# Kernel optimization log

Measured on AMD Instinct MI355X. Metric: run time of the kernel, lower is better.

Reference implementation:

```python
import jax, jax.numpy as jnp
import numpy as np

H = 16          # n_heads
D_MODEL = 1024
DK = D_MODEL // H  # 64
N = 2048        # total tokens (module flattens batch*seq)
NEG = -1000000000.0


def setup_inputs() -> dict:
    key = jax.random.key(0)
    ks = jax.random.split(key, 12)
    s = 1.0 / np.sqrt(D_MODEL)
    inp = {
        "query": jax.random.normal(ks[0], (N, D_MODEL), jnp.float32),
        "key": jax.random.normal(ks[1], (N, D_MODEL), jnp.float32),
        "value": jax.random.normal(ks[2], (N, D_MODEL), jnp.float32),
        "mask": jax.random.randint(ks[3], (1, N), 0, 2, jnp.int32),
        "Wq": jax.random.normal(ks[4], (D_MODEL, D_MODEL), jnp.float32) * s,
        "bq": jax.random.normal(ks[5], (D_MODEL,), jnp.float32) * 0.01,
        "Wk": jax.random.normal(ks[6], (D_MODEL, D_MODEL), jnp.float32) * s,
        "bk": jax.random.normal(ks[7], (D_MODEL,), jnp.float32) * 0.01,
        "Wv": jax.random.normal(ks[8], (D_MODEL, D_MODEL), jnp.float32) * s,
        "bv": jax.random.normal(ks[9], (D_MODEL,), jnp.float32) * 0.01,
        "Wo": jax.random.normal(ks[10], (D_MODEL, D_MODEL), jnp.float32) * s,
        "bo": jax.random.normal(ks[11], (D_MODEL,), jnp.float32) * 0.01,
    }
    return inp


def reference(query, key, value, mask, Wq, bq, Wk, bk, Wv, bv, Wo, bo):
    # Linear projections (torch Linear: x @ W.T + b), then split heads: (N, d_model) -> (h, N, d_k)
    def split_heads(x):
        return x.reshape(-1, H, DK).transpose(1, 0, 2)

    q = split_heads(query @ Wq.T + bq)
    k = split_heads(key @ Wk.T + bk)
    v = split_heads(value @ Wv.T + bv)

    # scaled dot-product attention: scores (h, N, N)
    scores = jnp.einsum("hnd,hmd->hnm", q, k) / jnp.sqrt(jnp.asarray(DK, q.dtype))
    # mask: (1, N) --unsqueeze(1)--> (1, 1, N), broadcast over (h, N, N)
    scores = jnp.where(mask[None, :, :] == 0, jnp.asarray(NEG, scores.dtype), scores)
    p_attn = jax.nn.softmax(scores, axis=-1)  # dropout identity (eval mode)

    x = jnp.einsum("hnm,hmd->hnd", p_attn, v)  # (h, N, d_k)
    x = x.transpose(1, 0, 2).reshape(-1, H * DK)  # (N, d_model)
    out = x @ Wo.T + bo
    return (out, p_attn)
```

## Files before the change

kernel.cpp:

```cpp
#include <hip/hip_runtime.h>


#define NTOK 2048
#define DMODEL 1024
#define NHEAD 16
#define DKH 64

typedef __attribute__((ext_vector_type(8))) short bf16x8;
typedef __attribute__((ext_vector_type(4))) float f32x4;

#define WAITVMC(n)                                          \
  do {                                                      \
    asm volatile("s_waitcnt vmcnt(" n ")" ::: "memory");    \
    __builtin_amdgcn_sched_barrier(0);                      \
  } while (0)
#define BARRIER()                                           \
  do {                                                      \
    __builtin_amdgcn_s_barrier();                           \
    __builtin_amdgcn_sched_barrier(0);                      \
  } while (0)

__device__ __forceinline__ unsigned short f2bf(float x) {
  unsigned int u = __builtin_bit_cast(unsigned int, x);
  u += 0x7fffu + ((u >> 16) & 1u);
  return (unsigned short)(u >> 16);
}

__device__ __forceinline__ void gl16(const void* g, void* l) {
  __builtin_amdgcn_global_load_lds((const __attribute__((address_space(1))) void*)g,
                                   (__attribute__((address_space(3))) void*)l, 16, 0, 0);
}

template<int ROWS>
__device__ __forceinline__ void stage_async(const unsigned short* src, int ld,
                                            char* lds, int w, int lane) {
  constexpr int RPW = ROWS / 4;
#pragma unroll
  for (int i = 0; i < RPW / 8; ++i) {
    const int row = w * RPW + i * 8 + (lane >> 3);
    const unsigned short* g = src + (size_t)row * ld + (((lane & 7) ^ (row & 7)) * 8);
    gl16(g, lds + (size_t)(w * RPW + i * 8) * 128);
  }
}

__device__ __forceinline__ void stage_v(const unsigned short* src, char* lds, int w, int lane) {
#pragma unroll
  for (int i = 0; i < 4; ++i) {
    const int row = w * 16 + i * 4 + (lane >> 4);
    const int ck = lane & 15;
    const unsigned short* g = src + (size_t)row * NTOK + ((ck ^ (row & 7)) * 8);
    gl16(g, lds + (size_t)(w * 16 + i * 4) * 256);
  }
}

__device__ __forceinline__ bf16x8 ldsfrag(const char* lds, int r, int kb) {
  return *(const bf16x8*)(lds + r * 128 + (kb ^ ((r & 7) << 4)));
}
__device__ __forceinline__ bf16x8 ldsfrag256(const char* lds, int r, int kb) {
  return *(const bf16x8*)(lds + r * 256 + (kb ^ ((r & 7) << 4)));
}

struct CvtP {
  const float* src[7];
  unsigned short* dst[7];
  int n8[8];
  const int* mask;
  float* mbias;
};
__global__ __launch_bounds__(256) void cvt_all(CvtP P) {
  const int a = blockIdx.z;
  const int i = blockIdx.x * 256 + threadIdx.x;
  if (i >= P.n8[a]) return;
  if (a == 7) {
#pragma unroll
    for (int r = 0; r < 8; ++r) {
      int j = i * 8 + r;
      P.mbias[j] = P.mask[j] ? 0.0f : -1e30f;
    }
    return;
  }
  const float4* s = (const float4*)P.src[a];
  float4 v0 = s[i * 2], v1 = s[i * 2 + 1];
  ushort4 h0, h1;
  h0.x = f2bf(v0.x); h0.y = f2bf(v0.y); h0.z = f2bf(v0.z); h0.w = f2bf(v0.w);
  h1.x = f2bf(v1.x); h1.y = f2bf(v1.y); h1.z = f2bf(v1.z); h1.w = f2bf(v1.w);
  ((ushort4*)P.dst[a])[i * 2] = h0;
  ((ushort4*)P.dst[a])[i * 2 + 1] = h1;
}

struct GemmP2 {
  const unsigned short* A[3];
  const unsigned short* B[3];
  const float* bias[3];
  unsigned short* Cb16;
  float* Cf32;
  unsigned short* VTd;
  long long sC;
  int lda, ldb, ldc, Nn, K;
};

template<int BM, bool OUTF32, bool VTRANS>
__global__ __launch_bounds__(256) void gemm_glds(GemmP2 P) {
  constexpr int BN = 128, WN = 64, FN = 4;
  constexpr int WM = BM / 2, FM = WM / 16;
  __shared__ char ldsA[BM * 128];
  __shared__ char ldsB[BN * 128];
  const int tid = threadIdx.x;
  const int lane = tid & 63, w = tid >> 6;
  const int l15 = lane & 15, lhi = lane >> 4;
  const int z = blockIdx.z;
  const int zi = (gridDim.z == 3) ? z : 0;
  const int ntn = P.Nn / BN;
  const int m0 = ((int)blockIdx.x / ntn) * BM;
  const int n0 = ((int)blockIdx.x % ntn) * BN;
  const unsigned short* Ab = P.A[zi] + (size_t)m0 * P.lda;
  const unsigned short* Bb = P.B[zi] + (size_t)n0 * P.ldb;
  const int wm = w >> 1, wn = w & 1;

  f32x4 acc[FM][FN] = {};
  for (int k0 = 0; k0 < P.K; k0 += 64) {
    stage_async<BM>(Ab + k0, P.lda, ldsA, w, lane);
    stage_async<BN>(Bb + k0, P.ldb, ldsB, w, lane);
    __syncthreads();
#pragma unroll
    for (int kk = 0; kk < 2; ++kk) {
      const int kb = kk * 64 + lhi * 16;
      bf16x8 a[FM], b[FN];
#pragma unroll
      for (int i = 0; i < FM; ++i) a[i] = ldsfrag(ldsA, wm * WM + i * 16 + l15, kb);
#pragma unroll
      for (int j = 0; j < FN; ++j) b[j] = ldsfrag(ldsB, wn * WN + j * 16 + l15, kb);
#pragma unroll
      for (int i = 0; i < FM; ++i)
#pragma unroll
        for (int j = 0; j < FN; ++j)
          acc[i][j] = __builtin_amdgcn_mfma_f32_16x16x32_bf16(a[i], b[j], acc[i][j], 0, 0, 0);
    }
    __syncthreads();
  }

  const int rbase = m0 + wm * WM + lhi * 4;
  const int cbase = n0 + wn * WN + l15;
  if (VTRANS && z == 2) {
#pragma unroll
    for (int j = 0; j < FN; ++j) {
      const int col = cbase + j * 16;
      const float badd = P.bias[zi][col];
#pragma unroll
      for (int i = 0; i < FM; ++i) {
        ushort4 t;
        t.x = f2bf(acc[i][j][0] + badd); t.y = f2bf(acc[i][j][1] + badd);
        t.z = f2bf(acc[i][j][2] + badd); t.w = f2bf(acc[i][j][3] + badd);
        *(ushort4*)(P.VTd + (size_t)col * NTOK + rbase + i * 16) = t;
      }
    }
    return;
  }
#pragma unroll
  for (int j = 0; j < FN; ++j) {
    const int col = cbase + j * 16;
    const float badd = P.bias[zi] ? P.bias[zi][col] : 0.0f;
#pragma unroll
    for (int i = 0; i < FM; ++i) {
#pragma unroll
      for (int rg = 0; rg < 4; ++rg) {
        const int row = rbase + i * 16 + rg;
        const float v = acc[i][j][rg] + badd;
        if constexpr (OUTF32)
          P.Cf32[(size_t)row * P.ldc + col] = v;
        else
          P.Cb16[(size_t)z * P.sC + (size_t)row * P.ldc + col] = f2bf(v);
      }
    }
  }
}

__global__ __launch_bounds__(256) void attn5(const unsigned short* __restrict__ QP,
                                             const unsigned short* __restrict__ KP,
                                             const unsigned short* __restrict__ VT,
                                             const float* __restrict__ mbias,
                                             float* __restrict__ p,
                                             unsigned short* __restrict__ XB) {
  __shared__ char ldsK[2][128 * 128];
  __shared__ char ldsV[2][64 * 256];
  __shared__ char ldsP[64 * 256];
  const int tid = threadIdx.x;
  const int lane = tid & 63, w = tid >> 6;
  const int l15 = lane & 15, lhi = lane >> 4;
  const int id = blockIdx.x;
  const int h = 2 * (id & 7) + ((id >> 3) & 1);
  const int q0 = (id >> 4) * 64;
  const int mrow = w * 16 + l15;
  constexpr float CEXP = 0.1803368801111204f;

  stage_async<64>(QP + (size_t)q0 * DMODEL + h * DKH, DMODEL, ldsP, w, lane);
  __syncthreads();
  bf16x8 qf0 = ldsfrag(ldsP, mrow, lhi * 16);
  bf16x8 qf1 = ldsfrag(ldsP, mrow, 64 + lhi * 16);

  const unsigned short* Kh = KP + h * DKH;
  const unsigned short* Vh = VT + (size_t)h * DKH * NTOK;

  float rsum = 0.0f;
  stage_async<128>(Kh, DMODEL, ldsK[0], w, lane);
  int b = 0;
  for (int it = 0; it < 16; ++it) {
    WAITVMC("0");
    BARRIER();
    if (it < 15)
      stage_async<128>(Kh + (size_t)(it + 1) * 128 * DMODEL, DMODEL, ldsK[b ^ 1], w, lane);
    __builtin_amdgcn_sched_barrier(0);
    f32x4 sacc[8] = {};
#pragma unroll
    for (int kk = 0; kk < 2; ++kk)
#pragma unroll
      for (int js = 0; js < 8; ++js) {
        bf16x8 kf = ldsfrag(ldsK[b], js * 16 + l15, kk * 64 + lhi * 16);
        sacc[js] = __builtin_amdgcn_mfma_f32_16x16x32_bf16(kf, kk ? qf1 : qf0, sacc[js], 0, 0, 0);
      }
    const float* mb = mbias + it * 128;
#pragma unroll
    for (int js = 0; js < 8; ++js) {
      float4 m4 = *(const float4*)(mb + js * 16 + lhi * 4);
      rsum += exp2f(sacc[js][0] * CEXP + m4.x);
      rsum += exp2f(sacc[js][1] * CEXP + m4.y);
      rsum += exp2f(sacc[js][2] * CEXP + m4.z);
      rsum += exp2f(sacc[js][3] * CEXP + m4.w);
    }
    b ^= 1;
  }
  rsum += __shfl_xor(rsum, 16, 64);
  rsum += __shfl_xor(rsum, 32, 64);
  const float lr = -log2f(rsum);

  f32x4 xacc[4] = {};
  stage_async<128>(Kh, DMODEL, ldsK[0], w, lane);
  stage_v(Vh, ldsV[0], w, lane);
  b = 0;
  for (int it = 0; it < 16; ++it) {
    const int j0 = it * 128;
    if (it == 0) { WAITVMC("0"); } else { WAITVMC("8"); }
    BARRIER();
    if (it < 15) {
      stage_async<128>(Kh + (size_t)(j0 + 128) * DMODEL, DMODEL, ldsK[b ^ 1], w, lane);
      stage_v(Vh + j0 + 128, ldsV[b ^ 1], w, lane);
    }
    __builtin_amdgcn_sched_barrier(0);
    f32x4 sacc[8] = {};
#pragma unroll
    for (int kk = 0; kk < 2; ++kk)
#pragma unroll
      for (int js = 0; js < 8; ++js) {
        bf16x8 kf = ldsfrag(ldsK[b], js * 16 + l15, kk * 64 + lhi * 16);
        sacc[js] = __builtin_amdgcn_mfma_f32_16x16x32_bf16(kf, kk ? qf1 : qf0, sacc[js], 0, 0, 0);
      }
    const float* mb = mbias + j0;
#pragma unroll
    for (int js = 0; js < 8; ++js) {
      float4 m4 = *(const float4*)(mb + js * 16 + lhi * 4);
      ushort4 pb;
      pb.x = f2bf(exp2f(sacc[js][0] * CEXP + (m4.x + lr)));
      pb.y = f2bf(exp2f(sacc[js][1] * CEXP + (m4.y + lr)));
      pb.z = f2bf(exp2f(sacc[js][2] * CEXP + (m4.z + lr)));
      pb.w = f2bf(exp2f(sacc[js][3] * CEXP + (m4.w + lr)));
      *(ushort4*)(ldsP + mrow * 256 + ((js * 32 + lhi * 8) ^ ((mrow & 7) << 4))) = pb;
    }
#pragma unroll
    for (int r = 0; r < 8; ++r) {
      const int row = w * 16 + r * 2 + (lane >> 5);
      const uint2 u =
          *(const uint2*)(ldsP + row * 256 + (((lane & 31) * 8) ^ ((row & 7) << 4)));
      f32x4 f;
      f[0] = __builtin_bit_cast(float, u.x << 16);
      f[1] = __builtin_bit_cast(float, u.x & 0xffff0000u);
      f[2] = __builtin_bit_cast(float, u.y << 16);
      f[3] = __builtin_bit_cast(float, u.y & 0xffff0000u);
      __builtin_nontemporal_store(
          f, (f32x4*)(p + ((size_t)h * NTOK + q0 + row) * NTOK + j0 + (lane & 31) * 4));
    }
#pragma unroll
    for (int jk = 0; jk < 4; ++jk) {
      bf16x8 pf = ldsfrag256(ldsP, mrow, jk * 64 + lhi * 16);
#pragma unroll
      for (int dd = 0; dd < 4; ++dd) {
        bf16x8 vf = ldsfrag256(ldsV[b], dd * 16 + l15, jk * 64 + lhi * 16);
        xacc[dd] = __builtin_amdgcn_mfma_f32_16x16x32_bf16(vf, pf, xacc[dd], 0, 0, 0);
      }
    }
    b ^= 1;
  }

  unsigned short* xrow = XB + (size_t)(q0 + mrow) * DMODEL + h * DKH;
#pragma unroll
  for (int dd = 0; dd < 4; ++dd) {
    ushort4 xb;
    xb.x = f2bf(xacc[dd][0]); xb.y = f2bf(xacc[dd][1]);
    xb.z = f2bf(xacc[dd][2]); xb.w = f2bf(xacc[dd][3]);
    *(ushort4*)(xrow + dd * 16 + lhi * 4) = xb;
  }
}

extern "C" void kernel_launch(void* const* d_in, const int* in_sizes, int n_in,
                              void* d_out, int out_size, void* d_ws, size_t ws_size,
                              hipStream_t stream) {
  (void)in_sizes; (void)n_in; (void)out_size; (void)ws_size;
  const float* query = (const float*)d_in[0];
  const float* key_  = (const float*)d_in[1];
  const float* value = (const float*)d_in[2];
  const int*   mask  = (const int*)d_in[3];
  const float* Wq = (const float*)d_in[4];
  const float* bq = (const float*)d_in[5];
  const float* Wk = (const float*)d_in[6];
  const float* bk = (const float*)d_in[7];
  const float* Wv = (const float*)d_in[8];
  const float* bv = (const float*)d_in[9];
  const float* Wo = (const float*)d_in[10];
  const float* bo = (const float*)d_in[11];

  float* out = (float*)d_out;
  float* p = out + (size_t)NTOK * DMODEL;

  char* ws = (char*)d_ws;
  unsigned short* QP  = (unsigned short*)(ws);
  unsigned short* KP  = (unsigned short*)(ws + (4u << 20));
  unsigned short* VT  = (unsigned short*)(ws + (8u << 20));
  unsigned short* XB  = (unsigned short*)(ws + (12u << 20));
  unsigned short* qB  = (unsigned short*)(ws + (16u << 20));
  unsigned short* kB  = (unsigned short*)(ws + (20u << 20));
  unsigned short* vB  = (unsigned short*)(ws + (24u << 20));
  unsigned short* WqB = (unsigned short*)(ws + (28u << 20));
  unsigned short* WkB = (unsigned short*)(ws + (30u << 20));
  unsigned short* WvB = (unsigned short*)(ws + (32u << 20));
  unsigned short* WoB = (unsigned short*)(ws + (34u << 20));
  float* mbias = (float*)(ws + (36u << 20));

  {
    CvtP C = {};
    C.src[0] = query; C.dst[0] = qB;  C.n8[0] = NTOK * DMODEL / 8;
    C.src[1] = key_;  C.dst[1] = kB;  C.n8[1] = NTOK * DMODEL / 8;
    C.src[2] = value; C.dst[2] = vB;  C.n8[2] = NTOK * DMODEL / 8;
    C.src[3] = Wq;    C.dst[3] = WqB; C.n8[3] = DMODEL * DMODEL / 8;
    C.src[4] = Wk;    C.dst[4] = WkB; C.n8[4] = DMODEL * DMODEL / 8;
    C.src[5] = Wv;    C.dst[5] = WvB; C.n8[5] = DMODEL * DMODEL / 8;
    C.src[6] = Wo;    C.dst[6] = WoB; C.n8[6] = DMODEL * DMODEL / 8;
    C.n8[7] = NTOK / 8;
    C.mask = mask; C.mbias = mbias;
    cvt_all<<<dim3(1024, 1, 8), 256, 0, stream>>>(C);
  }
  {
    GemmP2 P = {};
    P.A[0] = qB; P.A[1] = kB; P.A[2] = vB;
    P.B[0] = WqB; P.B[1] = WkB; P.B[2] = WvB;
    P.bias[0] = bq; P.bias[1] = bk; P.bias[2] = bv;
    P.Cb16 = QP; P.VTd = VT; P.sC = (long long)NTOK * DMODEL;
    P.lda = DMODEL; P.ldb = DMODEL; P.ldc = DMODEL; P.Nn = DMODEL; P.K = DMODEL;
    gemm_glds<128, false, true>
        <<<dim3((NTOK / 128) * (DMODEL / 128), 1, 3), 256, 0, stream>>>(P);
  }
  attn5<<<dim3(512), 256, 0, stream>>>(QP, KP, VT, mbias, p, XB);
  {
    GemmP2 P = {};
    P.A[0] = XB; P.B[0] = WoB; P.bias[0] = bo;
    P.Cf32 = out; P.sC = 0;
    P.lda = DMODEL; P.ldb = DMODEL; P.ldc = DMODEL; P.Nn = DMODEL; P.K = DMODEL;
    gemm_glds<64, true, false>
        <<<dim3((NTOK / 64) * (DMODEL / 128), 1, 1), 256, 0, stream>>>(P);
  }
}
```

Measured before the change: 147.1 us.

## Store attention probabilities directly from registers and prefetch mask bias before MFMAs

The attention kernel now writes the fp32 softmax probabilities straight from the exp results in registers with nontemporal stores. Before, it read bf16 values back from LDS, widened them and wrote coalesced rows. This removes an LDS read pass and stores full-precision probabilities, but each store now covers only 16 bytes per lane across scattered rows, so global coalescing is worse. The mask-bias loads are also hoisted ahead of the MFMA loop so their latency overlaps the matrix math.

```diff
diff --git a/kernel.cpp b/kernel.cpp
--- a/kernel.cpp
+++ b/kernel.cpp
@@ -175,7 +175,7 @@
   }
 }
 
-__global__ __launch_bounds__(256) void attn5(const unsigned short* __restrict__ QP,
+__global__ __launch_bounds__(256) void attn6(const unsigned short* __restrict__ QP,
                                              const unsigned short* __restrict__ KP,
                                              const unsigned short* __restrict__ VT,
                                              const float* __restrict__ mbias,
@@ -210,6 +210,10 @@
     if (it < 15)
       stage_async<128>(Kh + (size_t)(it + 1) * 128 * DMODEL, DMODEL, ldsK[b ^ 1], w, lane);
     __builtin_amdgcn_sched_barrier(0);
+    const float* mb = mbias + it * 128;
+    float4 m4s[8];
+#pragma unroll
+    for (int js = 0; js < 8; ++js) m4s[js] = *(const float4*)(mb + js * 16 + lhi * 4);
     f32x4 sacc[8] = {};
 #pragma unroll
     for (int kk = 0; kk < 2; ++kk)
@@ -218,14 +222,12 @@
         bf16x8 kf = ldsfrag(ldsK[b], js * 16 + l15, kk * 64 + lhi * 16);
         sacc[js] = __builtin_amdgcn_mfma_f32_16x16x32_bf16(kf, kk ? qf1 : qf0, sacc[js], 0, 0, 0);
       }
-    const float* mb = mbias + it * 128;
 #pragma unroll
     for (int js = 0; js < 8; ++js) {
-      float4 m4 = *(const float4*)(mb + js * 16 + lhi * 4);
-      rsum += exp2f(sacc[js][0] * CEXP + m4.x);
-      rsum += exp2f(sacc[js][1] * CEXP + m4.y);
-      rsum += exp2f(sacc[js][2] * CEXP + m4.z);
-      rsum += exp2f(sacc[js][3] * CEXP + m4.w);
+      rsum += exp2f(sacc[js][0] * CEXP + m4s[js].x);
+      rsum += exp2f(sacc[js][1] * CEXP + m4s[js].y);
+      rsum += exp2f(sacc[js][2] * CEXP + m4s[js].z);
+      rsum += exp2f(sacc[js][3] * CEXP + m4s[js].w);
     }
     b ^= 1;
   }
@@ -234,6 +236,7 @@
   const float lr = -log2f(rsum);
 
   f32x4 xacc[4] = {};
+  float* prow = p + ((size_t)h * NTOK + q0 + mrow) * NTOK;
   stage_async<128>(Kh, DMODEL, ldsK[0], w, lane);
   stage_v(Vh, ldsV[0], w, lane);
   b = 0;
@@ -246,6 +249,10 @@
       stage_v(Vh + j0 + 128, ldsV[b ^ 1], w, lane);
     }
     __builtin_amdgcn_sched_barrier(0);
+    const float* mb = mbias + j0;
+    float4 m4s[8];
+#pragma unroll
+    for (int js = 0; js < 8; ++js) m4s[js] = *(const float4*)(mb + js * 16 + lhi * 4);
     f32x4 sacc[8] = {};
 #pragma unroll
     for (int kk = 0; kk < 2; ++kk)
@@ -254,29 +261,17 @@
         bf16x8 kf = ldsfrag(ldsK[b], js * 16 + l15, kk * 64 + lhi * 16);
         sacc[js] = __builtin_amdgcn_mfma_f32_16x16x32_bf16(kf, kk ? qf1 : qf0, sacc[js], 0, 0, 0);
       }
-    const float* mb = mbias + j0;
 #pragma unroll
     for (int js = 0; js < 8; ++js) {
-      float4 m4 = *(const float4*)(mb + js * 16 + lhi * 4);
+      f32x4 e;
+      e[0] = exp2f(sacc[js][0] * CEXP + (m4s[js].x + lr));
+      e[1] = exp2f(sacc[js][1] * CEXP + (m4s[js].y + lr));
+      e[2] = exp2f(sacc[js][2] * CEXP + (m4s[js].z + lr));
+      e[3] = exp2f(sacc[js][3] * CEXP + (m4s[js].w + lr));
+      __builtin_nontemporal_store(e, (f32x4*)(prow + j0 + js * 16 + lhi * 4));
       ushort4 pb;
-      pb.x = f2bf(exp2f(sacc[js][0] * CEXP + (m4.x + lr)));
-      pb.y = f2bf(exp2f(sacc[js][1] * CEXP + (m4.y + lr)));
-      pb.z = f2bf(exp2f(sacc[js][2] * CEXP + (m4.z + lr)));
-      pb.w = f2bf(exp2f(sacc[js][3] * CEXP + (m4.w + lr)));
+      pb.x = f2bf(e[0]); pb.y = f2bf(e[1]); pb.z = f2bf(e[2]); pb.w = f2bf(e[3]);
       *(ushort4*)(ldsP + mrow * 256 + ((js * 32 + lhi * 8) ^ ((mrow & 7) << 4))) = pb;
-    }
-#pragma unroll
-    for (int r = 0; r < 8; ++r) {
-      const int row = w * 16 + r * 2 + (lane >> 5);
-      const uint2 u =
-          *(const uint2*)(ldsP + row * 256 + (((lane & 31) * 8) ^ ((row & 7) << 4)));
-      f32x4 f;
-      f[0] = __builtin_bit_cast(float, u.x << 16);
-      f[1] = __builtin_bit_cast(float, u.x & 0xffff0000u);
-      f[2] = __builtin_bit_cast(float, u.y << 16);
-      f[3] = __builtin_bit_cast(float, u.y & 0xffff0000u);
-      __builtin_nontemporal_store(
-          f, (f32x4*)(p + ((size_t)h * NTOK + q0 + row) * NTOK + j0 + (lane & 31) * 4));
     }
 #pragma unroll
     for (int jk = 0; jk < 4; ++jk) {
@@ -357,7 +352,7 @@
     gemm_glds<128, false, true>
         <<<dim3((NTOK / 128) * (DMODEL / 128), 1, 3), 256, 0, stream>>>(P);
   }
-  attn5<<<dim3(512), 256, 0, stream>>>(QP, KP, VT, mbias, p, XB);
+  attn6<<<dim3(512), 256, 0, stream>>>(QP, KP, VT, mbias, p, XB);
   {
     GemmP2 P = {};
     P.A[0] = XB; P.B[0] = WoB; P.bias[0] = bo;
```

New measurement: 185.5 us. 1.26x slower.

## Split attention key range across two wave groups with 512-thread blocks

Applied to the files above, without the earlier changes.

The attention kernel now runs 512 threads per block. Two groups of four waves each handle half of the key sequence, using 64-key tiles instead of 128. Row sums are combined through LDS before normalization, and the partial PV accumulators are reduced through LDS at the end. Mask-bias loads are prefetched one iteration ahead, and the P tile store is moved after the PV MFMAs. This doubles the waves per query tile to raise latency hiding and occupancy, at the cost of extra barriers and an LDS reduction.

```diff
diff --git a/kernel.cpp b/kernel.cpp
--- a/kernel.cpp
+++ b/kernel.cpp
@@ -43,21 +43,8 @@
   }
 }
 
-__device__ __forceinline__ void stage_v(const unsigned short* src, char* lds, int w, int lane) {
-#pragma unroll
-  for (int i = 0; i < 4; ++i) {
-    const int row = w * 16 + i * 4 + (lane >> 4);
-    const int ck = lane & 15;
-    const unsigned short* g = src + (size_t)row * NTOK + ((ck ^ (row & 7)) * 8);
-    gl16(g, lds + (size_t)(w * 16 + i * 4) * 256);
-  }
-}
-
 __device__ __forceinline__ bf16x8 ldsfrag(const char* lds, int r, int kb) {
   return *(const bf16x8*)(lds + r * 128 + (kb ^ ((r & 7) << 4)));
-}
-__device__ __forceinline__ bf16x8 ldsfrag256(const char* lds, int r, int kb) {
-  return *(const bf16x8*)(lds + r * 256 + (kb ^ ((r & 7) << 4)));
 }
 
 struct CvtP {
@@ -175,128 +162,173 @@
   }
 }
 
-__global__ __launch_bounds__(256) void attn5(const unsigned short* __restrict__ QP,
-                                             const unsigned short* __restrict__ KP,
-                                             const unsigned short* __restrict__ VT,
-                                             const float* __restrict__ mbias,
-                                             float* __restrict__ p,
-                                             unsigned short* __restrict__ XB) {
-  __shared__ char ldsK[2][128 * 128];
-  __shared__ char ldsV[2][64 * 256];
-  __shared__ char ldsP[64 * 256];
+__global__ __launch_bounds__(512, 4) void attn7(const unsigned short* __restrict__ QP,
+                                                const unsigned short* __restrict__ KP,
+                                                const unsigned short* __restrict__ VT,
+                                                const float* __restrict__ mbias,
+                                                float* __restrict__ p,
+                                                unsigned short* __restrict__ XB) {
+  __shared__ char ldsK[2][2][64 * 128];
+  __shared__ char ldsV[2][2][64 * 128];
+  __shared__ char ldsP[2][64 * 128];
   const int tid = threadIdx.x;
   const int lane = tid & 63, w = tid >> 6;
+  const int wm = w & 3, jg = w >> 2;
   const int l15 = lane & 15, lhi = lane >> 4;
   const int id = blockIdx.x;
   const int h = 2 * (id & 7) + ((id >> 3) & 1);
   const int q0 = (id >> 4) * 64;
-  const int mrow = w * 16 + l15;
+  const int mrow = wm * 16 + l15;
   constexpr float CEXP = 0.1803368801111204f;
 
-  stage_async<64>(QP + (size_t)q0 * DMODEL + h * DKH, DMODEL, ldsP, w, lane);
+  {
+    const int row = w * 8 + (lane >> 3);
+    const unsigned short* g =
+        QP + (size_t)(q0 + row) * DMODEL + h * DKH + (((lane & 7) ^ (row & 7)) * 8);
+    gl16(g, ldsP[0] + (size_t)(w * 8) * 128);
+  }
   __syncthreads();
-  bf16x8 qf0 = ldsfrag(ldsP, mrow, lhi * 16);
-  bf16x8 qf1 = ldsfrag(ldsP, mrow, 64 + lhi * 16);
-
-  const unsigned short* Kh = KP + h * DKH;
-  const unsigned short* Vh = VT + (size_t)h * DKH * NTOK;
+  bf16x8 qf0 = ldsfrag(ldsP[0], mrow, lhi * 16);
+  bf16x8 qf1 = ldsfrag(ldsP[0], mrow, 64 + lhi * 16);
+
+  const unsigned short* Kh = KP + (size_t)(jg * 1024) * DMODEL + h * DKH;
+  const unsigned short* Vh = VT + (size_t)h * DKH * NTOK + jg * 1024;
+  const float* mbh = mbias + jg * 1024;
 
   float rsum = 0.0f;
-  stage_async<128>(Kh, DMODEL, ldsK[0], w, lane);
+  stage_async<64>(Kh, DMODEL, ldsK[jg][0], wm, lane);
+  float4 m4n[4];
+#pragma unroll
+  for (int js = 0; js < 4; ++js) m4n[js] = *(const float4*)(mbh + js * 16 + lhi * 4);
   int b = 0;
   for (int it = 0; it < 16; ++it) {
     WAITVMC("0");
     BARRIER();
     if (it < 15)
-      stage_async<128>(Kh + (size_t)(it + 1) * 128 * DMODEL, DMODEL, ldsK[b ^ 1], w, lane);
+      stage_async<64>(Kh + (size_t)(it + 1) * 64 * DMODEL, DMODEL, ldsK[jg][b ^ 1], wm, lane);
+    float4 m4c[4];
+#pragma unroll
+    for (int js = 0; js < 4; ++js) m4c[js] = m4n[js];
+    if (it < 15) {
+      const float* mb = mbh + (it + 1) * 64;
+#pragma unroll
+      for (int js = 0; js < 4; ++js) m4n[js] = *(const float4*)(mb + js * 16 + lhi * 4);
+    }
     __builtin_amdgcn_sched_barrier(0);
-    f32x4 sacc[8] = {};
+    f32x4 sacc[4] = {};
 #pragma unroll
     for (int kk = 0; kk < 2; ++kk)
 #pragma unroll
-      for (int js = 0; js < 8; ++js) {
-        bf16x8 kf = ldsfrag(ldsK[b], js * 16 + l15, kk * 64 + lhi * 16);
+      for (int js = 0; js < 4; ++js) {
+        bf16x8 kf = ldsfrag(ldsK[jg][b], js * 16 + l15, kk * 64 + lhi * 16);
         sacc[js] = __builtin_amdgcn_mfma_f32_16x16x32_bf16(kf, kk ? qf1 : qf0, sacc[js], 0, 0, 0);
       }
-    const float* mb = mbias + it * 128;
-#pragma unroll
-    for (int js = 0; js < 8; ++js) {
-      float4 m4 = *(const float4*)(mb + js * 16 + lhi * 4);
-      rsum += exp2f(sacc[js][0] * CEXP + m4.x);
-      rsum += exp2f(sacc[js][1] * CEXP + m4.y);
-      rsum += exp2f(sacc[js][2] * CEXP + m4.z);
-      rsum += exp2f(sacc[js][3] * CEXP + m4.w);
+#pragma unroll
+    for (int js = 0; js < 4; ++js) {
+      rsum += exp2f(sacc[js][0] * CEXP + m4c[js].x);
+      rsum += exp2f(sacc[js][1] * CEXP + m4c[js].y);
+      rsum += exp2f(sacc[js][2] * CEXP + m4c[js].z);
+      rsum += exp2f(sacc[js][3] * CEXP + m4c[js].w);
     }
     b ^= 1;
   }
   rsum += __shfl_xor(rsum, 16, 64);
   rsum += __shfl_xor(rsum, 32, 64);
-  const float lr = -log2f(rsum);
+
+  float* ldsR = (float*)ldsP[0];
+  BARRIER();
+  if (lane < 16) ldsR[jg * 64 + mrow] = rsum;
+  BARRIER();
+  const float rtot = ldsR[mrow] + ldsR[64 + mrow];
+  const float lr = -log2f(rtot);
 
   f32x4 xacc[4] = {};
-  stage_async<128>(Kh, DMODEL, ldsK[0], w, lane);
-  stage_v(Vh, ldsV[0], w, lane);
+  stage_async<64>(Kh, DMODEL, ldsK[jg][0], wm, lane);
+  stage_async<64>(Vh, NTOK, ldsV[jg][0], wm, lane);
+#pragma unroll
+  for (int js = 0; js < 4; ++js) m4n[js] = *(const float4*)(mbh + js * 16 + lhi * 4);
   b = 0;
   for (int it = 0; it < 16; ++it) {
-    const int j0 = it * 128;
-    if (it == 0) { WAITVMC("0"); } else { WAITVMC("8"); }
+    const int j0 = it * 64;
+    if (it == 0) { WAITVMC("0"); } else { WAITVMC("4"); }
     BARRIER();
     if (it < 15) {
-      stage_async<128>(Kh + (size_t)(j0 + 128) * DMODEL, DMODEL, ldsK[b ^ 1], w, lane);
-      stage_v(Vh + j0 + 128, ldsV[b ^ 1], w, lane);
+      stage_async<64>(Kh + (size_t)(j0 + 64) * DMODEL, DMODEL, ldsK[jg][b ^ 1], wm, lane);
+      stage_async<64>(Vh + j0 + 64, NTOK, ldsV[jg][b ^ 1], wm, lane);
+    }
+    float4 m4c[4];
+#pragma unroll
+    for (int js = 0; js < 4; ++js) m4c[js] = m4n[js];
+    if (it < 15) {
+      const float* mb = mbh + (it + 1) * 64;
+#pragma unroll
+      for (int js = 0; js < 4; ++js) m4n[js] = *(const float4*)(mb + js * 16 + lhi * 4);
     }
     __builtin_amdgcn_sched_barrier(0);
-    f32x4 sacc[8] = {};
+    f32x4 sacc[4] = {};
 #pragma unroll
     for (int kk = 0; kk < 2; ++kk)
 #pragma unroll
-      for (int js = 0; js < 8; ++js) {
-        bf16x8 kf = ldsfrag(ldsK[b], js * 16 + l15, kk * 64 + lhi * 16);
+      for (int js = 0; js < 4; ++js) {
+        bf16x8 kf = ldsfrag(ldsK[jg][b], js * 16 + l15, kk * 64 + lhi * 16);
         sacc[js] = __builtin_amdgcn_mfma_f32_16x16x32_bf16(kf, kk ? qf1 : qf0, sacc[js], 0, 0, 0);
       }
-    const float* mb = mbias + j0;
-#pragma unroll
-    for (int js = 0; js < 8; ++js) {
-      float4 m4 = *(const float4*)(mb + js * 16 + lhi * 4);
+#pragma unroll
+    for (int js = 0; js < 4; ++js) {
+      f32x4 e;
+      e[0] = exp2f(sacc[js][0] * CEXP + (m4c[js].x + lr));
+      e[1] = exp2f(sacc[js][1] * CEXP + (m4c[js].y + lr));
+      e[2] = exp2f(sacc[js][2] * CEXP + (m4c[js].z + lr));
+      e[3] = exp2f(sacc[js][3] * CEXP + (m4c[js].w + lr));
       ushort4 pb;
-      pb.x = f2bf(exp2f(sacc[js][0] * CEXP + (m4.x + lr)));
-      pb.y = f2bf(exp2f(sacc[js][1] * CEXP + (m4.y + lr)));
-      pb.z = f2bf(exp2f(sacc[js][2] * CEXP + (m4.z + lr)));
-      pb.w = f2bf(exp2f(sacc[js][3] * CEXP + (m4.w + lr)));
-      *(ushort4*)(ldsP + mrow * 256 + ((js * 32 + lhi * 8) ^ ((mrow & 7) << 4))) = pb;
-    }
-#pragma unroll
-    for (int r = 0; r < 8; ++r) {
-      const int row = w * 16 + r * 2 + (lane >> 5);
+      pb.x = f2bf(e[0]); pb.y = f2bf(e[1]); pb.z = f2bf(e[2]); pb.w = f2bf(e[3]);
+      *(ushort4*)(ldsP[jg] + mrow * 128 + ((js * 32 + lhi * 8) ^ ((mrow & 7) << 4))) = pb;
+    }
+#pragma unroll
+    for (int jk = 0; jk < 2; ++jk) {
+      bf16x8 pf = ldsfrag(ldsP[jg], mrow, jk * 64 + lhi * 16);
+#pragma unroll
+      for (int dd = 0; dd < 4; ++dd) {
+        bf16x8 vf = ldsfrag(ldsV[jg][b], dd * 16 + l15, jk * 64 + lhi * 16);
+        xacc[dd] = __builtin_amdgcn_mfma_f32_16x16x32_bf16(vf, pf, xacc[dd], 0, 0, 0);
+      }
+    }
+#pragma unroll
+    for (int r = 0; r < 4; ++r) {
+      const int row = wm * 16 + r * 4 + lhi;
       const uint2 u =
-          *(const uint2*)(ldsP + row * 256 + (((lane & 31) * 8) ^ ((row & 7) << 4)));
+          *(const uint2*)(ldsP[jg] + row * 128 + ((l15 * 8) ^ ((row & 7) << 4)));
       f32x4 f;
       f[0] = __builtin_bit_cast(float, u.x << 16);
       f[1] = __builtin_bit_cast(float, u.x & 0xffff0000u);
       f[2] = __builtin_bit_cast(float, u.y << 16);
       f[3] = __builtin_bit_cast(float, u.y & 0xffff0000u);
       __builtin_nontemporal_store(
-          f, (f32x4*)(p + ((size_t)h * NTOK + q0 + row) * NTOK + j0 + (lane & 31) * 4));
-    }
-#pragma unroll
-    for (int jk = 0; jk < 4; ++jk) {
-      bf16x8 pf = ldsfrag256(ldsP, mrow, jk * 64 + lhi * 16);
-#pragma unroll
-      for (int dd = 0; dd < 4; ++dd) {
-        bf16x8 vf = ldsfrag256(ldsV[b], dd * 16 + l15, jk * 64 + lhi * 16);
-        xacc[dd] = __builtin_amdgcn_mfma_f32_16x16x32_bf16(vf, pf, xacc[dd], 0, 0, 0);
-      }
+          f, (f32x4*)(p + ((size_t)h * NTOK + q0 + row) * NTOK + jg * 1024 + j0 + l15 * 4));
     }
     b ^= 1;
   }
 
-  unsigned short* xrow = XB + (size_t)(q0 + mrow) * DMODEL + h * DKH;
-#pragma unroll
-  for (int dd = 0; dd < 4; ++dd) {
-    ushort4 xb;
-    xb.x = f2bf(xacc[dd][0]); xb.y = f2bf(xacc[dd][1]);
-    xb.z = f2bf(xacc[dd][2]); xb.w = f2bf(xacc[dd][3]);
-    *(ushort4*)(xrow + dd * 16 + lhi * 4) = xb;
+  float* ldsX = (float*)ldsK;
+  BARRIER();
+  if (jg == 1) {
+#pragma unroll
+    for (int dd = 0; dd < 4; ++dd) {
+      const int off = (mrow * 256 + ((dd * 64 + lhi * 16) ^ ((mrow & 7) << 4))) >> 2;
+      *(f32x4*)(ldsX + off) = xacc[dd];
+    }
+  }
+  BARRIER();
+  if (jg == 0) {
+    unsigned short* xrow = XB + (size_t)(q0 + mrow) * DMODEL + h * DKH;
+#pragma unroll
+    for (int dd = 0; dd < 4; ++dd) {
+      const int off = (mrow * 256 + ((dd * 64 + lhi * 16) ^ ((mrow & 7) << 4))) >> 2;
+      f32x4 o = xacc[dd] + *(const f32x4*)(ldsX + off);
+      ushort4 xb;
+      xb.x = f2bf(o[0]); xb.y = f2bf(o[1]); xb.z = f2bf(o[2]); xb.w = f2bf(o[3]);
+      *(ushort4*)(xrow + dd * 16 + lhi * 4) = xb;
+    }
   }
 }
 
@@ -357,7 +389,7 @@
     gemm_glds<128, false, true>
         <<<dim3((NTOK / 128) * (DMODEL / 128), 1, 3), 256, 0, stream>>>(P);
   }
-  attn5<<<dim3(512), 256, 0, stream>>>(QP, KP, VT, mbias, p, XB);
+  attn7<<<dim3(512), 512, 0, stream>>>(QP, KP, VT, mbias, p, XB);
   {
     GemmP2 P = {};
     P.A[0] = XB; P.B[0] = WoB; P.bias[0] = bo;
```

New measurement: 148.2 us (median of 2 runs). About the same (+0.7%).
